# Kernel tuning notes

Measured on AMD Instinct MI355X. Metric: run time of the kernel, lower is better.

The kernel has to match this reference:

```python
import jax, jax.numpy as jnp
import numpy as np

B, S, E, H = 2, 2048, 1024, 16
D = E // H  # head_dim = 64

def setup_inputs() -> dict:
    key = jax.random.key(0)
    k1, k2, k3 = jax.random.split(key, 3)
    x = jax.random.normal(k1, (B, S, E), dtype=jnp.float32)
    W_attn = jax.random.normal(k2, (E, 3 * E), dtype=jnp.float32) * 0.02
    b_attn = jnp.zeros((3 * E,), dtype=jnp.float32)
    W_proj = jax.random.normal(k3, (E, E), dtype=jnp.float32) * 0.02
    b_proj = jnp.zeros((E,), dtype=jnp.float32)
    return {"x": x, "W_attn": W_attn, "b_attn": b_attn, "W_proj": W_proj, "b_proj": b_proj}

def reference(x, W_attn, b_attn, W_proj, b_proj):
    bsz, seq, emb = x.shape
    # fused QKV projection (Conv1D == linear with [in,out] weight)
    qkv = x @ W_attn + b_attn                       # [B,S,3E]
    q, k, v = jnp.split(qkv, 3, axis=-1)
    def to_heads(t):
        return t.reshape(bsz, seq, H, D).transpose(0, 2, 1, 3)  # [B,H,S,D]
    q, k, v = to_heads(q), to_heads(k), to_heads(v)
    scale = jnp.float32(D) ** -0.5
    scores = jnp.einsum('bhqd,bhkd->bhqk', q, k) * scale        # [B,H,S,S]
    causal = jnp.tril(jnp.ones((seq, seq), dtype=bool))
    scores = jnp.where(causal, scores, jnp.float32(-jnp.inf))
    attn = jax.nn.softmax(scores, axis=-1)
    out = jnp.einsum('bhqk,bhkd->bhqd', attn, v)                # [B,H,S,D]
    out = out.transpose(0, 2, 1, 3).reshape(bsz, seq, emb)
    y = out @ W_proj + b_proj
    return y
```

## Files before the change

### kernel.cpp

```cpp
#include <hip/hip_runtime.h>
#include <hip/hip_bf16.h>


typedef __bf16 bf16;
typedef __bf16 bf16x4 __attribute__((ext_vector_type(4)));
typedef __bf16 bf16x8 __attribute__((ext_vector_type(8)));
typedef float  f32x4  __attribute__((ext_vector_type(4)));

#define MNEG (-1.0e30f)
#define QSCALE 0.1803368801f

__device__ __forceinline__ void gload16(const bf16* g, bf16* l) {
  __builtin_amdgcn_global_load_lds((const __attribute__((address_space(1))) void*)g,
                                   (__attribute__((address_space(3))) void*)l, 16, 0, 0);
}

__global__ __launch_bounds__(256) void prep_k(const float* __restrict__ x, bf16* __restrict__ xb,
                                              const float* __restrict__ Wa, bf16* __restrict__ WaT,
                                              const float* __restrict__ Wp, bf16* __restrict__ WpT) {
  const int bid = blockIdx.x;
  if (bid < 2048) {
    const int i = bid * 256 + threadIdx.x;
    f32x4 a = ((const f32x4*)x)[2 * i], b = ((const f32x4*)x)[2 * i + 1];
    bf16x8 o;
    for (int j = 0; j < 4; ++j) { o[j] = (bf16)a[j]; o[4 + j] = (bf16)b[j]; }
    ((bf16x8*)xb)[i] = o;
    return;
  }
  __shared__ bf16 t[64][68];
  const float* in; bf16* out; int C, cx, cy;
  if (bid < 2816) { in = Wa; out = WaT; C = 3072; const int tt = bid - 2048; cx = tt % 48; cy = tt / 48; }
  else            { in = Wp; out = WpT; C = 1024; const int tt = bid - 2816; cx = tt % 16; cy = tt / 16; }
  const int R = 1024;
  const int c0 = cx * 64, r0 = cy * 64;
  const int lr = threadIdx.x >> 4;
  const int lc = (threadIdx.x & 15) * 4;
  for (int i = 0; i < 4; ++i) {
    int r = lr + i * 16;
    f32x4 v = *(const f32x4*)(in + (size_t)(r0 + r) * C + c0 + lc);
    bf16x4 b;
    for (int j = 0; j < 4; ++j) b[j] = (bf16)v[j];
    *(bf16x4*)&t[r][lc] = b;
  }
  __syncthreads();
  for (int i = 0; i < 4; ++i) {
    int c = lr + i * 16;
    bf16x4 v;
    for (int j = 0; j < 4; ++j) v[j] = t[lc + j][c];
    *(bf16x4*)(out + (size_t)(c0 + c) * R + r0 + lc) = v;
  }
}

template <int MODE, int BN>
__global__ __launch_bounds__(256) void gemm_bt(const bf16* __restrict__ A,
                                               const bf16* __restrict__ Bt,
                                               const float* __restrict__ bias,
                                               float* __restrict__ C,
                                               bf16* __restrict__ Qo,
                                               bf16* __restrict__ Ko,
                                               bf16* __restrict__ Vo,
                                               int M, int N, int K) {
  constexpr int NT = BN / 32;
  __shared__ bf16 As[128 * 32];
  __shared__ bf16 Bs[BN * 32];
  const int tid = threadIdx.x;
  const int w = tid >> 6, l = tid & 63;
  const int nx = gridDim.x;
  const int nwg = nx * gridDim.y;
  const int flat = blockIdx.y * nx + blockIdx.x;
  const int swz = (flat & 7) * (nwg >> 3) + (flat >> 3);
  const int m0 = (swz / nx) * 128, n0 = (swz % nx) * BN;
  const int wm = w >> 1, wn = w & 1;
  const int fr = l & 15, fg = l >> 4;
  const int srow = l >> 2;
  const int scol = (l & 3) * 8;

  f32x4 acc[4][NT] = {};

  for (int k0 = 0; k0 < K; k0 += 32) {
    __syncthreads();
    for (int c = 0; c < 2; ++c) {
      const int rowA = 32 * w + 16 * c + srow;
      gload16(A + (size_t)(m0 + rowA) * K + k0 + scol, As + (32 * w + 16 * c) * 32);
    }
    for (int c = 0; c < BN / 64; ++c) {
      const int rb = (BN / 64) * 16 * w + 16 * c;
      gload16(Bt + (size_t)(n0 + rb + srow) * K + k0 + scol, Bs + rb * 32);
    }
    __syncthreads();

    bf16x8 af[4], bfv[NT];
    for (int mt = 0; mt < 4; ++mt)
      af[mt] = *(const bf16x8*)(As + (wm * 64 + mt * 16 + fr) * 32 + 8 * fg);
    for (int nt = 0; nt < NT; ++nt)
      bfv[nt] = *(const bf16x8*)(Bs + (wn * (BN / 2) + nt * 16 + fr) * 32 + 8 * fg);
    for (int mt = 0; mt < 4; ++mt)
      for (int nt = 0; nt < NT; ++nt)
        acc[mt][nt] = __builtin_amdgcn_mfma_f32_16x16x32_bf16(af[mt], bfv[nt], acc[mt][nt], 0, 0, 0);
  }

  for (int mt = 0; mt < 4; ++mt) {
    for (int nt = 0; nt < NT; ++nt) {
      const int row0 = m0 + wm * 64 + mt * 16 + 4 * fg;
      const int col = n0 + wn * (BN / 2) + nt * 16 + fr;
      const float bv = bias[col];
      if (MODE == 0) {
        for (int r = 0; r < 4; ++r)
          C[(size_t)(row0 + r) * N + col] = acc[mt][nt][r] + bv;
      } else {
        const int which = col >> 10, h = (col >> 6) & 15, d = col & 63;
        const int b = row0 >> 11, s = row0 & 2047;
        if (which == 2) {
          bf16x4 vv;
          for (int r = 0; r < 4; ++r) vv[r] = (bf16)(acc[mt][nt][r] + bv);
          *(bf16x4*)(Vo + ((size_t)(b * 16 + h) * 64 + d) * 2048 + s) = vv;
        } else if (which == 0) {
          for (int r = 0; r < 4; ++r)
            Qo[((size_t)(b * 16 + h) * 2048 + s + r) * 64 + d] =
                (bf16)((acc[mt][nt][r] + bv) * QSCALE);
        } else {
          for (int r = 0; r < 4; ++r)
            Ko[((size_t)(b * 16 + h) * 2048 + s + r) * 64 + d] = (bf16)(acc[mt][nt][r] + bv);
        }
      }
    }
  }
}

__global__ __launch_bounds__(128) void attn_k(const bf16* __restrict__ Qw,
                                              const bf16* __restrict__ Kw,
                                              const bf16* __restrict__ VtG,
                                              bf16* __restrict__ AO) {
  __shared__ bf16 Ks[64 * 72];
  __shared__ bf16 Vt[64 * 72];
  __shared__ bf16 Ps[2 * 16 * 72];
  const int tid = threadIdx.x, w = tid >> 6, l = tid & 63;
  const int flat = blockIdx.x;
  const int bh = (flat & 7) + 8 * (flat >> 8);
  const int xp = (flat >> 3) & 31;
  const int qa0 = xp * 32;
  const int qb0 = (63 - xp) * 32;
  const int fr = l & 15, fg = l >> 4;
  const size_t base = (size_t)bh * 2048 * 64;
  const int qaw = qa0 + w * 16, qbw = qb0 + w * 16;
  const int qa = qaw + fr, qb = qbw + fr;
  const int ktmax_a = ((qa0 + 31) >> 6) << 6;
  const int ktmax_b = ((qb0 + 31) >> 6) << 6;
  bf16* Pw = Ps + w * 16 * 72;
  const int scol8 = (tid & 7) * 8;

  bf16x8 qfa[2], qfb[2];
  for (int t = 0; t < 2; ++t) {
    qfa[t] = *(const bf16x8*)(Qw + base + (size_t)(qaw + fr) * 64 + 32 * t + 8 * fg);
    qfb[t] = *(const bf16x8*)(Qw + base + (size_t)(qbw + fr) * 64 + 32 * t + 8 * fg);
  }

  f32x4 oa[4] = {}, ob[4] = {};
  float la = 0.f, lb = 0.f;
  bf16x8 kreg[4], vreg[4];

  auto load_tile = [&](int kt) {
    for (int c = 0; c < 4; ++c) {
      const int row = (tid >> 3) + 16 * c;
      kreg[c] = *(const bf16x8*)(Kw + base + (size_t)(kt + row) * 64 + scol8);
      vreg[c] = *(const bf16x8*)(VtG + base + (size_t)row * 2048 + kt + scol8);
    }
  };
  auto write_tile = [&]() {
    for (int c = 0; c < 4; ++c) {
      const int row = (tid >> 3) + 16 * c;
      *(bf16x8*)(Ks + row * 72 + scol8) = kreg[c];
      *(bf16x8*)(Vt + row * 72 + scol8) = vreg[c];
    }
  };

  auto smpv = [&](f32x4 (&sc)[4], f32x4 (&oacc)[4], float& lsum,
                  int q, bool need_mask, int kt) {
    float psum = 0.f;
    for (int c = 0; c < 4; ++c) {
      bf16x4 pb;
      for (int r = 0; r < 4; ++r) {
        float s = sc[c][r];
        if (need_mask && (kt + c * 16 + 4 * fg + r > q)) s = MNEG;
        const float p = __builtin_amdgcn_exp2f(s);
        psum += p;
        pb[r] = (bf16)p;
      }
      *(bf16x4*)(Pw + fr * 72 + c * 16 + 4 * fg) = pb;
    }
    psum += __shfl_xor(psum, 16, 64);
    psum += __shfl_xor(psum, 32, 64);
    lsum += psum;
    asm volatile("" ::: "memory");
    __builtin_amdgcn_s_setprio(1);
    for (int t = 0; t < 2; ++t) {
      bf16x8 pa = *(const bf16x8*)(Pw + fr * 72 + 32 * t + 8 * fg);
      for (int dt = 0; dt < 4; ++dt) {
        bf16x8 vf = *(const bf16x8*)(Vt + (dt * 16 + fr) * 72 + 32 * t + 8 * fg);
        oacc[dt] = __builtin_amdgcn_mfma_f32_16x16x32_bf16(pa, vf, oacc[dt], 0, 0, 0);
      }
    }
    __builtin_amdgcn_s_setprio(0);
    asm volatile("" ::: "memory");
  };

  load_tile(0);
  write_tile();
  __syncthreads();

  for (int kt = 0; kt <= ktmax_b; kt += 64) {
    const bool havenext = (kt + 64 <= ktmax_b);
    if (havenext) load_tile(kt + 64);

    const bool doA = (kt <= ktmax_a);
    f32x4 sa[4], sb[4];
    __builtin_amdgcn_s_setprio(1);
    for (int c = 0; c < 4; ++c) {
      bf16x8 kf0 = *(const bf16x8*)(Ks + (c * 16 + fr) * 72 + 8 * fg);
      bf16x8 kf1 = *(const bf16x8*)(Ks + (c * 16 + fr) * 72 + 32 + 8 * fg);
      f32x4 z = {};
      z = __builtin_amdgcn_mfma_f32_16x16x32_bf16(kf0, qfb[0], z, 0, 0, 0);
      sb[c] = __builtin_amdgcn_mfma_f32_16x16x32_bf16(kf1, qfb[1], z, 0, 0, 0);
      if (doA) {
        f32x4 y = {};
        y = __builtin_amdgcn_mfma_f32_16x16x32_bf16(kf0, qfa[0], y, 0, 0, 0);
        sa[c] = __builtin_amdgcn_mfma_f32_16x16x32_bf16(kf1, qfa[1], y, 0, 0, 0);
      }
    }
    __builtin_amdgcn_s_setprio(0);
    if (doA) smpv(sa, oa, la, qa, kt + 63 > qaw, kt);
    smpv(sb, ob, lb, qb, kt + 63 > qbw, kt);

    if (!havenext) break;
    __syncthreads();
    write_tile();
    __syncthreads();
  }

  const int b = bh >> 4, h = bh & 15;
  auto store = [&](const f32x4 (&oacc)[4], float l2, int qw0) {
    float linv[4];
    for (int r = 0; r < 4; ++r)
      linv[r] = 1.f / __shfl(l2, (l & 48) | (4 * fg + r), 64);
    for (int dt = 0; dt < 4; ++dt)
      for (int r = 0; r < 4; ++r) {
        const int qq = qw0 + 4 * fg + r;
        AO[(size_t)(b * 2048 + qq) * 1024 + h * 64 + dt * 16 + fr] =
            (bf16)(oacc[dt][r] * linv[r]);
      }
  };
  store(oa, la, qaw);
  store(ob, lb, qbw);
}

extern "C" void kernel_launch(void* const* d_in, const int* in_sizes, int n_in,
                              void* d_out, int out_size, void* d_ws, size_t ws_size,
                              hipStream_t stream) {
  const float* x      = (const float*)d_in[0];
  const float* W_attn = (const float*)d_in[1];
  const float* b_attn = (const float*)d_in[2];
  const float* W_proj = (const float*)d_in[3];
  const float* b_proj = (const float*)d_in[4];
  float* out = (float*)d_out;

  char* ws = (char*)d_ws;
  bf16* WaT = (bf16*)(ws);
  bf16* WpT = (bf16*)(ws + 6291456);
  bf16* Qw  = (bf16*)(ws + 8388608);
  bf16* Kw  = (bf16*)(ws + 16777216);
  bf16* VtG = (bf16*)(ws + 25165824);
  bf16* AO  = (bf16*)(ws + 33554432);
  bf16* xb  = AO;

  prep_k<<<3072, 256, 0, stream>>>(x, xb, W_attn, WaT, W_proj, WpT);

  gemm_bt<1, 128><<<dim3(24, 32), 256, 0, stream>>>(
      xb, WaT, b_attn, nullptr, Qw, Kw, VtG, 4096, 3072, 1024);

  attn_k<<<1024, 128, 0, stream>>>(Qw, Kw, VtG, AO);

  gemm_bt<0, 64><<<dim3(16, 32), 256, 0, stream>>>(
      AO, WpT, b_proj, out, nullptr, nullptr, nullptr, 4096, 1024, 1024);
}
```

Before: 128.2 us.

## Enlarge attention blocks to 4 waves with 64-row query pairs and 128-key tiles

The attention kernel now runs 256 threads per block, each block covering two 64-row query strips (a balanced causal pair) instead of two 32-row strips, and stages 128 keys per shared-memory tile processed as two 64-key halves. This halves the grid, doubles K/V reuse per staged tile, and halves the number of barrier pairs per key range. Separate P buffers per strip remove the compiler memory fences. The cost is more shared memory per block, fewer blocks (512) to fill the CUs, and coarser causal granularity that can do extra masked work on the last tile.

```diff
diff --git a/kernel.cpp b/kernel.cpp
--- a/kernel.cpp
+++ b/kernel.cpp
@@ -127,27 +127,28 @@
   }
 }
 
-__global__ __launch_bounds__(128) void attn_k(const bf16* __restrict__ Qw,
+__global__ __launch_bounds__(256) void attn_k(const bf16* __restrict__ Qw,
                                               const bf16* __restrict__ Kw,
                                               const bf16* __restrict__ VtG,
                                               bf16* __restrict__ AO) {
-  __shared__ bf16 Ks[64 * 72];
-  __shared__ bf16 Vt[64 * 72];
-  __shared__ bf16 Ps[2 * 16 * 72];
+  __shared__ bf16 Ks[128 * 72];
+  __shared__ bf16 Vt[64 * 136];
+  __shared__ bf16 Psa[4 * 16 * 72];
+  __shared__ bf16 Psb[4 * 16 * 72];
   const int tid = threadIdx.x, w = tid >> 6, l = tid & 63;
-  const int flat = blockIdx.x;
-  const int bh = (flat & 7) + 8 * (flat >> 8);
-  const int xp = (flat >> 3) & 31;
-  const int qa0 = xp * 32;
-  const int qb0 = (63 - xp) * 32;
+  const int bid = blockIdx.x;
+  const int bh = ((bid & 7) << 2) | ((bid >> 3) & 3);
+  const int xp = bid >> 5;
+  const int qa0 = xp * 64;
+  const int qb0 = (31 - xp) * 64;
   const int fr = l & 15, fg = l >> 4;
   const size_t base = (size_t)bh * 2048 * 64;
   const int qaw = qa0 + w * 16, qbw = qb0 + w * 16;
   const int qa = qaw + fr, qb = qbw + fr;
-  const int ktmax_a = ((qa0 + 31) >> 6) << 6;
-  const int ktmax_b = ((qb0 + 31) >> 6) << 6;
-  bf16* Pw = Ps + w * 16 * 72;
-  const int scol8 = (tid & 7) * 8;
+  bf16* Pwa = Psa + w * 16 * 72;
+  bf16* Pwb = Psb + w * 16 * 72;
+  const int r8 = tid >> 3, c8 = (tid & 7) * 8;
+  const int r16 = tid >> 4, c16 = (tid & 15) * 8;
 
   bf16x8 qfa[2], qfb[2];
   for (int t = 0; t < 2; ++t) {
@@ -161,27 +162,25 @@
 
   auto load_tile = [&](int kt) {
     for (int c = 0; c < 4; ++c) {
-      const int row = (tid >> 3) + 16 * c;
-      kreg[c] = *(const bf16x8*)(Kw + base + (size_t)(kt + row) * 64 + scol8);
-      vreg[c] = *(const bf16x8*)(VtG + base + (size_t)row * 2048 + kt + scol8);
+      kreg[c] = *(const bf16x8*)(Kw + base + (size_t)(kt + r8 + 32 * c) * 64 + c8);
+      vreg[c] = *(const bf16x8*)(VtG + base + (size_t)(r16 + 16 * c) * 2048 + kt + c16);
     }
   };
   auto write_tile = [&]() {
     for (int c = 0; c < 4; ++c) {
-      const int row = (tid >> 3) + 16 * c;
-      *(bf16x8*)(Ks + row * 72 + scol8) = kreg[c];
-      *(bf16x8*)(Vt + row * 72 + scol8) = vreg[c];
-    }
-  };
-
-  auto smpv = [&](f32x4 (&sc)[4], f32x4 (&oacc)[4], float& lsum,
-                  int q, bool need_mask, int kt) {
+      *(bf16x8*)(Ks + (r8 + 32 * c) * 72 + c8) = kreg[c];
+      *(bf16x8*)(Vt + (r16 + 16 * c) * 136 + c16) = vreg[c];
+    }
+  };
+
+  auto smpv = [&](f32x4 (&sc)[4], bf16* Pw, f32x4 (&oacc)[4], float& lsum,
+                  int q, bool need_mask, int kh, int h) {
     float psum = 0.f;
     for (int c = 0; c < 4; ++c) {
       bf16x4 pb;
       for (int r = 0; r < 4; ++r) {
         float s = sc[c][r];
-        if (need_mask && (kt + c * 16 + 4 * fg + r > q)) s = MNEG;
+        if (need_mask && (kh + c * 16 + 4 * fg + r > q)) s = MNEG;
         const float p = __builtin_amdgcn_exp2f(s);
         psum += p;
         pb[r] = (bf16)p;
@@ -191,45 +190,47 @@
     psum += __shfl_xor(psum, 16, 64);
     psum += __shfl_xor(psum, 32, 64);
     lsum += psum;
-    asm volatile("" ::: "memory");
     __builtin_amdgcn_s_setprio(1);
     for (int t = 0; t < 2; ++t) {
       bf16x8 pa = *(const bf16x8*)(Pw + fr * 72 + 32 * t + 8 * fg);
       for (int dt = 0; dt < 4; ++dt) {
-        bf16x8 vf = *(const bf16x8*)(Vt + (dt * 16 + fr) * 72 + 32 * t + 8 * fg);
+        bf16x8 vf = *(const bf16x8*)(Vt + (dt * 16 + fr) * 136 + 64 * h + 32 * t + 8 * fg);
         oacc[dt] = __builtin_amdgcn_mfma_f32_16x16x32_bf16(pa, vf, oacc[dt], 0, 0, 0);
       }
     }
     __builtin_amdgcn_s_setprio(0);
-    asm volatile("" ::: "memory");
   };
 
   load_tile(0);
   write_tile();
   __syncthreads();
 
-  for (int kt = 0; kt <= ktmax_b; kt += 64) {
-    const bool havenext = (kt + 64 <= ktmax_b);
-    if (havenext) load_tile(kt + 64);
-
-    const bool doA = (kt <= ktmax_a);
-    f32x4 sa[4], sb[4];
-    __builtin_amdgcn_s_setprio(1);
-    for (int c = 0; c < 4; ++c) {
-      bf16x8 kf0 = *(const bf16x8*)(Ks + (c * 16 + fr) * 72 + 8 * fg);
-      bf16x8 kf1 = *(const bf16x8*)(Ks + (c * 16 + fr) * 72 + 32 + 8 * fg);
-      f32x4 z = {};
-      z = __builtin_amdgcn_mfma_f32_16x16x32_bf16(kf0, qfb[0], z, 0, 0, 0);
-      sb[c] = __builtin_amdgcn_mfma_f32_16x16x32_bf16(kf1, qfb[1], z, 0, 0, 0);
-      if (doA) {
-        f32x4 y = {};
-        y = __builtin_amdgcn_mfma_f32_16x16x32_bf16(kf0, qfa[0], y, 0, 0, 0);
-        sa[c] = __builtin_amdgcn_mfma_f32_16x16x32_bf16(kf1, qfa[1], y, 0, 0, 0);
-      }
-    }
-    __builtin_amdgcn_s_setprio(0);
-    if (doA) smpv(sa, oa, la, qa, kt + 63 > qaw, kt);
-    smpv(sb, ob, lb, qb, kt + 63 > qbw, kt);
+  for (int kt = 0; kt <= qb0; kt += 128) {
+    const bool havenext = (kt + 128 <= qb0);
+    if (havenext) load_tile(kt + 128);
+
+    for (int h = 0; h < 2; ++h) {
+      const int kh = kt + 64 * h;
+      if (kh > qb0) break;
+      const bool doA = (kh <= qa0);
+      f32x4 sa[4], sb[4];
+      __builtin_amdgcn_s_setprio(1);
+      for (int c = 0; c < 4; ++c) {
+        bf16x8 kf0 = *(const bf16x8*)(Ks + (64 * h + c * 16 + fr) * 72 + 8 * fg);
+        bf16x8 kf1 = *(const bf16x8*)(Ks + (64 * h + c * 16 + fr) * 72 + 32 + 8 * fg);
+        f32x4 z = {};
+        z = __builtin_amdgcn_mfma_f32_16x16x32_bf16(kf0, qfb[0], z, 0, 0, 0);
+        sb[c] = __builtin_amdgcn_mfma_f32_16x16x32_bf16(kf1, qfb[1], z, 0, 0, 0);
+        if (doA) {
+          f32x4 y = {};
+          y = __builtin_amdgcn_mfma_f32_16x16x32_bf16(kf0, qfa[0], y, 0, 0, 0);
+          sa[c] = __builtin_amdgcn_mfma_f32_16x16x32_bf16(kf1, qfa[1], y, 0, 0, 0);
+        }
+      }
+      __builtin_amdgcn_s_setprio(0);
+      if (doA) smpv(sa, Pwa, oa, la, qa, kh + 63 > qaw, kh, h);
+      smpv(sb, Pwb, ob, lb, qb, kh + 63 > qbw, kh, h);
+    }
 
     if (!havenext) break;
     __syncthreads();
@@ -277,7 +278,7 @@
   gemm_bt<1, 128><<<dim3(24, 32), 256, 0, stream>>>(
       xb, WaT, b_attn, nullptr, Qw, Kw, VtG, 4096, 3072, 1024);
 
-  attn_k<<<1024, 128, 0, stream>>>(Qw, Kw, VtG, AO);
+  attn_k<<<512, 256, 0, stream>>>(Qw, Kw, VtG, AO);
 
   gemm_bt<0, 64><<<dim3(16, 32), 256, 0, stream>>>(
       AO, WpT, b_proj, out, nullptr, nullptr, nullptr, 4096, 1024, 1024);
```

New measurement: 120.9 us. -5.7%, faster.
